# Optimization experiments

Hardware: AMD Instinct MI355X
Metric: run time of the kernel (lower is better)

Reference implementation:

```python
import jax, jax.numpy as jnp
import numpy as np

NC, NP, NF, NI, NIND = 150000, 300000, 100000, 700, 500
D, H, P = 64, 64, 32768


def setup_inputs() -> dict:
    key = jax.random.key(0)
    ks = jax.random.split(key, 40)

    def nrm(k, shape, s=0.05):
        return jax.random.normal(k, shape, dtype=jnp.float32) * s

    def idx(k, shape, hi):
        return jax.random.randint(k, shape, 0, hi, dtype=jnp.int32)

    def msk(k, shape):
        m = jax.random.bernoulli(k, 0.7, shape)
        return m.at[:, 0].set(True)  # guarantee >=1 neighbor per node

    inp = {
        # paths: columns are (company, patent, first_patentee, patent) for 'cpfp'
        "paths": jnp.stack([idx(ks[0], (P,), NC), idx(ks[1], (P,), NP),
                             idx(ks[2], (P,), NF), idx(ks[3], (P,), NP)], axis=1),
        "label": (jax.random.uniform(ks[4], (P,)) > 0.5).astype(jnp.float32),
        "pat_fp_idx": idx(ks[5], (NP, 2), NF),   "pat_fp_mask": msk(ks[6], (NP, 2)),
        "pat_ipc_idx": idx(ks[7], (NP, 6), NI),  "pat_ipc_mask": msk(ks[8], (NP, 6)),
        "pat_comp_idx": idx(ks[9], (NP, 2), NC), "pat_comp_mask": msk(ks[10], (NP, 2)),
        "comp_ind_idx": idx(ks[11], (NC, 4), NIND), "comp_ind_mask": msk(ks[12], (NC, 4)),
        "comp_pat_idx": idx(ks[13], (NC, 16), NP),  "comp_pat_mask": msk(ks[14], (NC, 16)),
        # embedding tables
        "company_emb": nrm(ks[15], (NC, D)),
        "patent_emb": nrm(ks[16], (NP, D)),
        "fp_emb": nrm(ks[17], (NF, D)),
        "ipc_emb": nrm(ks[18], (NI, D)),
        "ind_emb": nrm(ks[19], (NIND, D)),
        # LSTM (torch gate order i,f,g,o)
        "W_ih": nrm(ks[20], (4 * H, D)), "W_hh": nrm(ks[21], (4 * H, H)),
        "b_ih": jnp.zeros((4 * H,), jnp.float32), "b_hh": jnp.zeros((4 * H,), jnp.float32),
        # att_mlp: Linear(2D,D) -> LeakyReLU(0.2) -> Linear(D,1) -> Sigmoid
        "att_W1": nrm(ks[22], (2 * D, D)), "att_b1": jnp.zeros((D,), jnp.float32),
        "att_W2": nrm(ks[23], (D, 1)),     "att_b2": jnp.zeros((1,), jnp.float32),
        # score mlp: Linear(H,H) -> ReLU -> Linear(H,1) -> Sigmoid
        "mlp_W1": nrm(ks[24], (H, H)), "mlp_b1": jnp.zeros((H,), jnp.float32),
        "mlp_W2": nrm(ks[25], (H, 1)), "mlp_b2": jnp.zeros((1,), jnp.float32),
    }
    return inp


def _masked_sum(tab, idx, mask):
    # tab [V,D], idx [N,K], mask [N,K] bool -> (sum [N,D], count [N])
    e = tab[idx] * mask[..., None].astype(tab.dtype)
    return e.sum(1), mask.sum(1).astype(tab.dtype)


def _att_fuse(e, sub, W1, b1, W2, b2):
    # entity_embedding + subgraph * att_mlp([entity, subgraph])
    h = jax.nn.leaky_relu(jnp.concatenate([e, sub], -1) @ W1 + b1, 0.2)
    w = jax.nn.sigmoid(h @ W2 + b2)  # [P,1]
    return e + sub * w


def _lstm_last(seq, W_ih, W_hh, b_ih, b_hh):
    # seq [P,T,D] -> last hidden [P,H]
    h0 = jnp.zeros((seq.shape[0], H), seq.dtype)
    c0 = jnp.zeros_like(h0)

    def step(carry, x):
        h, c = carry
        g = x @ W_ih.T + b_ih + h @ W_hh.T + b_hh
        i, f, gg, o = jnp.split(g, 4, axis=-1)
        c = jax.nn.sigmoid(f) * c + jax.nn.sigmoid(i) * jnp.tanh(gg)
        h = jax.nn.sigmoid(o) * jnp.tanh(c)
        return (h, c), None

    (h, _), _ = jax.lax.scan(step, (h0, c0), jnp.swapaxes(seq, 0, 1))
    return h


def reference(paths, label, pat_fp_idx, pat_fp_mask, pat_ipc_idx, pat_ipc_mask,
              pat_comp_idx, pat_comp_mask, comp_ind_idx, comp_ind_mask,
              comp_pat_idx, comp_pat_mask, company_emb, patent_emb, fp_emb,
              ipc_emb, ind_emb, W_ih, W_hh, b_ih, b_hh, att_W1, att_b1,
              att_W2, att_b2, mlp_W1, mlp_b1, mlp_W2, mlp_b2):
    # --- compute_subgraph_representation (aggregator='avg'), vectorized ---
    s1, c1 = _masked_sum(fp_emb, pat_fp_idx, pat_fp_mask)
    s2, c2 = _masked_sum(ipc_emb, pat_ipc_idx, pat_ipc_mask)
    s3, c3 = _masked_sum(company_emb, pat_comp_idx, pat_comp_mask)
    patent_sub = patent_emb + (s1 + s2 + s3) / (c1 + c2 + c3)[:, None]  # [NP,D]

    t1, d1 = _masked_sum(ind_emb, comp_ind_idx, comp_ind_mask)
    t2, d2 = _masked_sum(patent_emb, comp_pat_idx, comp_pat_mask)
    company_sub = company_emb + (t1 + t2) / (d1 + d2)[:, None]          # [NC,D]

    # --- per-path entity embeddings for 'cpfp' ---
    e0 = company_emb[paths[:, 0]]
    e1 = patent_emb[paths[:, 1]]
    e2 = fp_emb[paths[:, 2]]
    e3 = patent_emb[paths[:, 3]]

    # fusion_type='att': fuse company subgraph (head) and patent subgraph (tail)
    # into intermediate entities (positions 1 and 2), sequentially.
    csub = company_sub[paths[:, 0]]
    psub = patent_sub[paths[:, 3]]
    e1 = _att_fuse(_att_fuse(e1, csub, att_W1, att_b1, att_W2, att_b2),
                   psub, att_W1, att_b1, att_W2, att_b2)
    e2 = _att_fuse(_att_fuse(e2, csub, att_W1, att_b1, att_W2, att_b2),
                   psub, att_W1, att_b1, att_W2, att_b2)

    seq = jnp.stack([e0, e1, e2, e3], axis=1)  # [P,4,D]
    h = _lstm_last(seq, W_ih, W_hh, b_ih, b_hh)  # [P,H]
    score = jax.nn.sigmoid(jax.nn.relu(h @ mlp_W1 + mlp_b1) @ mlp_W2 + mlp_b2)
    return score[:, 0]  # [P]
```

## Files before the change

kernel.cpp:

```cpp
#include <hip/hip_runtime.h>
#include <stdint.h>

typedef unsigned short u16;
typedef unsigned short u16x8 __attribute__((ext_vector_type(8)));
typedef short s16x8 __attribute__((ext_vector_type(8)));
typedef float f32x4 __attribute__((ext_vector_type(4)));

__device__ __forceinline__ float b2f(u16 u){ return __uint_as_float(((unsigned)u)<<16); }
__device__ __forceinline__ u16 f2b(float f){
  unsigned u = __float_as_uint(f);
  u += 0x7FFF + ((u>>16)&1);
  return (u16)(u>>16);
}
__device__ __forceinline__ float sigm(float x){ return 1.0f/(1.0f+__expf(-x)); }
__device__ __forceinline__ float tanhf_(float x){ return 2.0f/(1.0f+__expf(-2.0f*x)) - 1.0f; }

__device__ __forceinline__ f32x4 mf(s16x8 a, s16x8 b, f32x4 c){
  return __builtin_amdgcn_mfma_f32_16x16x32_bf16(a, b, c, 0, 0, 0);
}

__global__ void prep_kernel(const float* __restrict__ att_W1, const float* __restrict__ W_ih,
                            const float* __restrict__ W_hh, const float* __restrict__ mlp_W1,
                            u16* __restrict__ pack){
  int t = blockIdx.x*blockDim.x + threadIdx.x;
  if (t >= 5632) return;
  int lane = t & 63;
  int kb = (lane>>4)<<3;
  int nl = lane & 15;
  u16x8 o;
  if (t < 1024){
    int f = t>>6; int nt=f>>2, ks=f&3;
    int n = (nt<<4)+nl;
    #pragma unroll
    for (int j=0;j<8;j++){ int k = ks*32+kb+j; o[j] = f2b(att_W1[k*64+n]); }
  } else if (t < 3072){
    int f=(t-1024)>>6; int nt=f>>1, ks=f&1;
    int n=(nt<<4)+nl;
    #pragma unroll
    for (int j=0;j<8;j++){ int k=ks*32+kb+j; o[j]=f2b(W_ih[n*64+k]); }
  } else if (t < 5120){
    int f=(t-3072)>>6; int nt=f>>1, ks=f&1;
    int n=(nt<<4)+nl;
    #pragma unroll
    for (int j=0;j<8;j++){ int k=ks*32+kb+j; o[j]=f2b(W_hh[n*64+k]); }
  } else {
    int f=(t-5120)>>6; int nt=f>>1, ks=f&1;
    int n=(nt<<4)+nl;
    #pragma unroll
    for (int j=0;j<8;j++){ int k=ks*32+kb+j; o[j]=f2b(mlp_W1[k*64+n]); }
  }
  ((u16x8*)pack)[t] = o;
}

__global__ __launch_bounds__(256) void gather_kernel(
    const int* __restrict__ paths,
    const int* __restrict__ pat_fp_idx,  const uint8_t* __restrict__ pat_fp_mask,
    const int* __restrict__ pat_ipc_idx, const uint8_t* __restrict__ pat_ipc_mask,
    const int* __restrict__ pat_comp_idx,const uint8_t* __restrict__ pat_comp_mask,
    const int* __restrict__ comp_ind_idx,const uint8_t* __restrict__ comp_ind_mask,
    const int* __restrict__ comp_pat_idx,const uint8_t* __restrict__ comp_pat_mask,
    const float* __restrict__ company_emb, const float* __restrict__ patent_emb,
    const float* __restrict__ fp_emb, const float* __restrict__ ipc_emb,
    const float* __restrict__ ind_emb,
    u16* __restrict__ tileimg, int P, int total)
{
  const int lane = threadIdx.x & 63;
  const int p = (blockIdx.x<<2) + (threadIdx.x>>6);
  if (p >= total) return;
  const int ps = p < P ? p : (P-1);
  const int4 pq = *(const int4*)&paths[ps*4];

  int4   ci  = *(const int4*)  &comp_ind_idx [pq.x*4];
  const uchar4 cim = *(const uchar4*)&comp_ind_mask[pq.x*4];
  ci.y = cim.y ? ci.y : ci.x;  ci.z = cim.z ? ci.z : ci.x;  ci.w = cim.w ? ci.w : ci.x;

  int4   cp[4]; uchar4 cpm[4];
  #pragma unroll
  for (int q=0;q<4;q++){
    cp[q]  = *(const int4*)  &comp_pat_idx [pq.x*16+q*4];
    cpm[q] = *(const uchar4*)&comp_pat_mask[pq.x*16+q*4];
  }
  const int cp0 = cp[0].x;
  #pragma unroll
  for (int q=0;q<4;q++){
    cp[q].x = cpm[q].x ? cp[q].x : cp0;  cp[q].y = cpm[q].y ? cp[q].y : cp0;
    cp[q].z = cpm[q].z ? cp[q].z : cp0;  cp[q].w = cpm[q].w ? cp[q].w : cp0;
  }

  int2   fi  = *(const int2*)  &pat_fp_idx  [pq.w*2];
  const uchar2 fim = *(const uchar2*)&pat_fp_mask [pq.w*2];
  fi.y = fim.y ? fi.y : fi.x;

  int2   ip[3]; uchar2 ipm[3];
  #pragma unroll
  for (int q=0;q<3;q++){
    ip[q]  = *(const int2*)  &pat_ipc_idx [pq.w*6+q*2];
    ipm[q] = *(const uchar2*)&pat_ipc_mask[pq.w*6+q*2];
  }
  const int ip0 = ip[0].x;
  #pragma unroll
  for (int q=0;q<3;q++){
    ip[q].x = ipm[q].x ? ip[q].x : ip0;  ip[q].y = ipm[q].y ? ip[q].y : ip0;
  }

  int2   cc  = *(const int2*)  &pat_comp_idx [pq.w*2];
  const uchar2 ccm = *(const uchar2*)&pat_comp_mask[pq.w*2];
  cc.y = ccm.y ? cc.y : cc.x;

  const float e0 = company_emb[(long)pq.x*64+lane];
  const float e1 = patent_emb [(long)pq.y*64+lane];
  const float e2 = fp_emb     [(long)pq.z*64+lane];
  const float e3 = patent_emb [(long)pq.w*64+lane];

  float vind[4];
  vind[0]=ind_emb[(long)ci.x*64+lane]; vind[1]=ind_emb[(long)ci.y*64+lane];
  vind[2]=ind_emb[(long)ci.z*64+lane]; vind[3]=ind_emb[(long)ci.w*64+lane];
  float vpat[16];
  #pragma unroll
  for (int q=0;q<4;q++){
    vpat[q*4+0]=patent_emb[(long)cp[q].x*64+lane];
    vpat[q*4+1]=patent_emb[(long)cp[q].y*64+lane];
    vpat[q*4+2]=patent_emb[(long)cp[q].z*64+lane];
    vpat[q*4+3]=patent_emb[(long)cp[q].w*64+lane];
  }
  float vfp[2];
  vfp[0]=fp_emb[(long)fi.x*64+lane]; vfp[1]=fp_emb[(long)fi.y*64+lane];
  float vipc[6];
  #pragma unroll
  for (int q=0;q<3;q++){
    vipc[q*2+0]=ipc_emb[(long)ip[q].x*64+lane];
    vipc[q*2+1]=ipc_emb[(long)ip[q].y*64+lane];
  }
  float vcc[2];
  vcc[0]=company_emb[(long)cc.x*64+lane]; vcc[1]=company_emb[(long)cc.y*64+lane];

  float mi[4] = {(float)cim.x,(float)cim.y,(float)cim.z,(float)cim.w};
  float mp[16];
  #pragma unroll
  for (int q=0;q<4;q++){ mp[q*4]=(float)cpm[q].x; mp[q*4+1]=(float)cpm[q].y; mp[q*4+2]=(float)cpm[q].z; mp[q*4+3]=(float)cpm[q].w; }
  float a0=0.f, a1=0.f, c0=0.f, c1=0.f;
  #pragma unroll
  for (int j=0;j<4;j++){ a0 = fmaf(mi[j], vind[j], a0); c0 += mi[j]; }
  #pragma unroll
  for (int j=0;j<16;j++){
    if (j&1){ a1 = fmaf(mp[j], vpat[j], a1); c1 += mp[j]; }
    else    { a0 = fmaf(mp[j], vpat[j], a0); c0 += mp[j]; }
  }
  const float csub = e0 + (a0+a1)/(c0+c1);

  float mf2[2] = {(float)fim.x,(float)fim.y};
  float mip[6];
  #pragma unroll
  for (int q=0;q<3;q++){ mip[q*2]=(float)ipm[q].x; mip[q*2+1]=(float)ipm[q].y; }
  float mcc[2] = {(float)ccm.x,(float)ccm.y};
  float b0=0.f, b1=0.f, d0=0.f, d1=0.f;
  #pragma unroll
  for (int j=0;j<2;j++){ b0 = fmaf(mf2[j], vfp[j], b0); d0 += mf2[j]; }
  #pragma unroll
  for (int j=0;j<6;j++){
    if (j&1){ b1 = fmaf(mip[j], vipc[j], b1); d1 += mip[j]; }
    else    { b0 = fmaf(mip[j], vipc[j], b0); d0 += mip[j]; }
  }
  #pragma unroll
  for (int j=0;j<2;j++){ b1 = fmaf(mcc[j], vcc[j], b1); d1 += mcc[j]; }
  const float psub = e3 + (b0+b1)/(d0+d1);

  const int tile = p>>4, r = p&15;
  const int sc = lane ^ ((r&7)<<3);
  u16* b = tileimg + ((size_t)tile*6*16 + r)*64 + sc;
  b[0*1024] = f2b(e0);   b[1*1024] = f2b(e1);   b[2*1024] = f2b(e2);
  b[3*1024] = f2b(e3);   b[4*1024] = f2b(csub); b[5*1024] = f2b(psub);
}

__global__ __launch_bounds__(64) void path_kernel_fast(
    const float* __restrict__ b_ih, const float* __restrict__ b_hh,
    const float* __restrict__ att_b1, const float* __restrict__ att_W2, const float* __restrict__ att_b2,
    const float* __restrict__ mlp_b1, const float* __restrict__ mlp_W2, const float* __restrict__ mlp_b2,
    const u16* __restrict__ pack, const u16* __restrict__ tileimg,
    float* __restrict__ out, int P)
{
  __shared__ __align__(16) u16 ldsT[6][16][64];
  __shared__ float wbuf[32];
  const int lane = threadIdx.x;
  const int tile = blockIdx.x;
  const int base = tile * 16;
  if (base >= P) return;
  const u16x8* pk8 = (const u16x8*)pack;

  const char* src = (const char*)(tileimg + (size_t)tile*6144);
  #pragma unroll
  for (int it=0; it<12; ++it){
    __builtin_amdgcn_global_load_lds(
      (const __attribute__((address_space(1))) uint32_t*)(src + it*1024 + lane*16),
      (__attribute__((address_space(3))) uint32_t*)((char*)&ldsT[0][0][0] + it*1024),
      16, 0, 0);
  }
  asm volatile("s_waitcnt vmcnt(0)" ::: "memory");
  __builtin_amdgcn_sched_barrier(0);

  auto ldA = [&](int t, int ks)->s16x8{
    int row = lane & 15;
    int off = (ks*32 + ((lane>>4)<<3)) ^ ((row&7)<<3);
    return *(const s16x8*)&ldsT[t][row][off];
  };

  float attb1v[4], attw2v[4];
  #pragma unroll
  for (int q=0;q<4;q++){ int c=(q<<4)+(lane&15); attb1v[q]=att_b1[c]; attw2v[q]=att_W2[c]; }
  const float attb2 = att_b2[0];

  auto fuse = [&](int st){
    s16x8 a1[4], a2[4];
    #pragma unroll
    for (int ks=0;ks<2;ks++){
      a1[ks]=ldA(1,ks); a2[ks]=ldA(2,ks);
      s16x8 asub=ldA(st,ks); a1[2+ks]=asub; a2[2+ks]=asub;
    }
    f32x4 c1[4], c2[4];
    #pragma unroll
    for (int nt=0;nt<4;nt++){
      f32x4 x1={0.f,0.f,0.f,0.f}, x2={0.f,0.f,0.f,0.f};
      #pragma unroll
      for (int ks=0;ks<4;ks++){
        s16x8 b = *(const s16x8*)&pk8[(nt*4+ks)*64 + lane];
        x1 = mf(a1[ks], b, x1);
        x2 = mf(a2[ks], b, x2);
      }
      c1[nt]=x1; c2[nt]=x2;
    }
    float t1[4]={0.f,0.f,0.f,0.f}, t2[4]={0.f,0.f,0.f,0.f};
    #pragma unroll
    for (int nt=0;nt<4;nt++){
      #pragma unroll
      for (int r=0;r<4;r++){
        float h1=c1[nt][r]+attb1v[nt]; h1 = h1>0.f?h1:0.2f*h1;
        float h2=c2[nt][r]+attb1v[nt]; h2 = h2>0.f?h2:0.2f*h2;
        t1[r] += h1*attw2v[nt]; t2[r] += h2*attw2v[nt];
      }
    }
    #pragma unroll
    for (int r=0;r<4;r++){
      #pragma unroll
      for (int off=1; off<16; off<<=1){ t1[r]+=__shfl_xor(t1[r],off,64); t2[r]+=__shfl_xor(t2[r],off,64); }
    }
    if ((lane&15)==0){
      int g = lane>>4;
      #pragma unroll
      for (int r=0;r<4;r++){ wbuf[g*4+r] = sigm(t1[r]+attb2); wbuf[16+g*4+r] = sigm(t2[r]+attb2); }
    }
    #pragma unroll
    for (int it=0; it<2; it++){
      int row = it*8 + (lane>>3);
      int off = ((lane&7)<<3) ^ ((row&7)<<3);
      u16x8 ue1 = *(const u16x8*)&ldsT[1][row][off];
      u16x8 ue2 = *(const u16x8*)&ldsT[2][row][off];
      u16x8 us  = *(const u16x8*)&ldsT[st][row][off];
      float wA = wbuf[row], wB = wbuf[16+row];
      u16x8 o1, o2;
      #pragma unroll
      for (int j=0;j<8;j++){
        float sv=b2f(us[j]);
        o1[j]=f2b(b2f(ue1[j]) + sv*wA);
        o2[j]=f2b(b2f(ue2[j]) + sv*wB);
      }
      *(u16x8*)&ldsT[1][row][off]=o1;
      *(u16x8*)&ldsT[2][row][off]=o2;
    }
  };
  fuse(4);
  fuse(5);

  float biasv[16];
  #pragma unroll
  for (int nt=0;nt<16;nt++){ int c=(nt<<4)+(lane&15); biasv[nt]=b_ih[c]+b_hh[c]; }
  float cst[16];
  #pragma unroll
  for (int i=0;i<16;i++) cst[i]=0.f;

  auto step=[&](int xt, bool useH){
    s16x8 ax0=ldA(xt,0), ax1=ldA(xt,1);
    s16x8 ah0, ah1;
    if (useH){ ah0=ldA(4,0); ah1=ldA(4,1); }
    f32x4 acc[16];
    #pragma unroll
    for (int nt=0;nt<16;nt++){
      f32x4 a={0.f,0.f,0.f,0.f};
      a = mf(ax0, *(const s16x8*)&pk8[1024 + (nt*2+0)*64 + lane], a);
      a = mf(ax1, *(const s16x8*)&pk8[1024 + (nt*2+1)*64 + lane], a);
      if (useH){
        a = mf(ah0, *(const s16x8*)&pk8[3072 + (nt*2+0)*64 + lane], a);
        a = mf(ah1, *(const s16x8*)&pk8[3072 + (nt*2+1)*64 + lane], a);
      }
      acc[nt]=a;
    }
    #pragma unroll
    for (int q=0;q<4;q++){
      #pragma unroll
      for (int r=0;r<4;r++){
        float iv=sigm  (acc[q    ][r]+biasv[q]);
        float fv=sigm  (acc[4+q  ][r]+biasv[4+q]);
        float gv=tanhf_(acc[8+q  ][r]+biasv[8+q]);
        float ov=sigm  (acc[12+q ][r]+biasv[12+q]);
        float cc=fv*cst[q*4+r]+iv*gv;
        cst[q*4+r]=cc;
        float hv=ov*tanhf_(cc);
        int row=((lane>>4)<<2)+r;
        int col=(lane&15)+(q<<4);
        ldsT[4][row][col ^ ((row&7)<<3)] = f2b(hv);
      }
    }
  };
  step(0,false); step(1,true); step(2,true); step(3,true);

  float mlb1v[4], mlw2v[4];
  #pragma unroll
  for (int q=0;q<4;q++){ int c=(q<<4)+(lane&15); mlb1v[q]=mlp_b1[c]; mlw2v[q]=mlp_W2[c]; }
  const float mlb2 = mlp_b2[0];
  s16x8 ah0=ldA(4,0), ah1=ldA(4,1);
  f32x4 mac[4];
  #pragma unroll
  for (int nt=0;nt<4;nt++){
    f32x4 a={0.f,0.f,0.f,0.f};
    a = mf(ah0, *(const s16x8*)&pk8[5120 + (nt*2+0)*64 + lane], a);
    a = mf(ah1, *(const s16x8*)&pk8[5120 + (nt*2+1)*64 + lane], a);
    mac[nt]=a;
  }
  float tt[4]={0.f,0.f,0.f,0.f};
  #pragma unroll
  for (int nt=0;nt<4;nt++){
    #pragma unroll
    for (int r=0;r<4;r++){ float mv=mac[nt][r]+mlb1v[nt]; mv=mv>0.f?mv:0.f; tt[r]+=mv*mlw2v[nt]; }
  }
  #pragma unroll
  for (int r=0;r<4;r++){
    #pragma unroll
    for (int off=1; off<16; off<<=1) tt[r]+=__shfl_xor(tt[r],off,64);
  }
  if ((lane&15)==0){
    #pragma unroll
    for (int r=0;r<4;r++){
      int p = base + ((lane>>4)<<2) + r;
      if (p < P) out[p] = sigm(tt[r]+mlb2);
    }
  }
}

__global__ __launch_bounds__(64) void path_kernel_fused(
    const int* __restrict__ paths,
    const int* __restrict__ pat_fp_idx,  const uint8_t* __restrict__ pat_fp_mask,
    const int* __restrict__ pat_ipc_idx, const uint8_t* __restrict__ pat_ipc_mask,
    const int* __restrict__ pat_comp_idx,const uint8_t* __restrict__ pat_comp_mask,
    const int* __restrict__ comp_ind_idx,const uint8_t* __restrict__ comp_ind_mask,
    const int* __restrict__ comp_pat_idx,const uint8_t* __restrict__ comp_pat_mask,
    const float* __restrict__ company_emb, const float* __restrict__ patent_emb,
    const float* __restrict__ fp_emb, const float* __restrict__ ipc_emb,
    const float* __restrict__ ind_emb,
    const float* __restrict__ b_ih, const float* __restrict__ b_hh,
    const float* __restrict__ att_b1, const float* __restrict__ att_W2, const float* __restrict__ att_b2,
    const float* __restrict__ mlp_b1, const float* __restrict__ mlp_W2, const float* __restrict__ mlp_b2,
    const u16* __restrict__ pack,
    float* __restrict__ out, int P)
{
  __shared__ __align__(16) u16 ldsT[7][16][64];
  __shared__ float wbuf[32];
  const int lane = threadIdx.x;
  const int base = blockIdx.x * 16;
  if (base >= P) return;
  const u16x8* pk8 = (const u16x8*)pack;

  #pragma unroll 2
  for (int r=0;r<16;r++){
    int p = base + r; int ps = p < P ? p : (P-1);
    const int4 pq = *(const int4*)&paths[ps*4];
    float e0 = company_emb[(long)pq.x*64+lane];
    float e1 = patent_emb [(long)pq.y*64+lane];
    float e2 = fp_emb     [(long)pq.z*64+lane];
    float e3 = patent_emb [(long)pq.w*64+lane];
    float acc=0.f, cnt=0.f;
    #pragma unroll
    for (int jj=0;jj<4;jj++)
      if (comp_ind_mask[pq.x*4+jj]) { acc += ind_emb[(long)comp_ind_idx[pq.x*4+jj]*64+lane]; cnt += 1.f; }
    #pragma unroll
    for (int jj=0;jj<16;jj++)
      if (comp_pat_mask[pq.x*16+jj]){ acc += patent_emb[(long)comp_pat_idx[pq.x*16+jj]*64+lane]; cnt += 1.f; }
    float csub = e0 + acc/cnt;
    acc=0.f; cnt=0.f;
    #pragma unroll
    for (int jj=0;jj<2;jj++)
      if (pat_fp_mask[pq.w*2+jj])  { acc += fp_emb[(long)pat_fp_idx[pq.w*2+jj]*64+lane]; cnt += 1.f; }
    #pragma unroll
    for (int jj=0;jj<6;jj++)
      if (pat_ipc_mask[pq.w*6+jj]) { acc += ipc_emb[(long)pat_ipc_idx[pq.w*6+jj]*64+lane]; cnt += 1.f; }
    #pragma unroll
    for (int jj=0;jj<2;jj++)
      if (pat_comp_mask[pq.w*2+jj]){ acc += company_emb[(long)pat_comp_idx[pq.w*2+jj]*64+lane]; cnt += 1.f; }
    float psub = e3 + acc/cnt;
    int sc = lane ^ ((r&7)<<3);
    ldsT[0][r][sc]=f2b(e0); ldsT[1][r][sc]=f2b(e1); ldsT[2][r][sc]=f2b(e2);
    ldsT[3][r][sc]=f2b(e3); ldsT[4][r][sc]=f2b(csub); ldsT[5][r][sc]=f2b(psub);
  }

  auto ldA = [&](int t, int ks)->s16x8{
    int row = lane & 15;
    int off = (ks*32 + ((lane>>4)<<3)) ^ ((row&7)<<3);
    return *(const s16x8*)&ldsT[t][row][off];
  };

  float attb1v[4], attw2v[4];
  #pragma unroll
  for (int q=0;q<4;q++){ int c=(q<<4)+(lane&15); attb1v[q]=att_b1[c]; attw2v[q]=att_W2[c]; }
  const float attb2 = att_b2[0];

  auto fuse = [&](int st){
    s16x8 a1[4], a2[4];
    #pragma unroll
    for (int ks=0;ks<2;ks++){
      a1[ks]=ldA(1,ks); a2[ks]=ldA(2,ks);
      s16x8 asub=ldA(st,ks); a1[2+ks]=asub; a2[2+ks]=asub;
    }
    f32x4 c1[4], c2[4];
    #pragma unroll
    for (int nt=0;nt<4;nt++){
      f32x4 x1={0.f,0.f,0.f,0.f}, x2={0.f,0.f,0.f,0.f};
      #pragma unroll
      for (int ks=0;ks<4;ks++){
        s16x8 b = *(const s16x8*)&pk8[(nt*4+ks)*64 + lane];
        x1 = mf(a1[ks], b, x1);
        x2 = mf(a2[ks], b, x2);
      }
      c1[nt]=x1; c2[nt]=x2;
    }
    float t1[4]={0.f,0.f,0.f,0.f}, t2[4]={0.f,0.f,0.f,0.f};
    #pragma unroll
    for (int nt=0;nt<4;nt++){
      #pragma unroll
      for (int r=0;r<4;r++){
        float h1=c1[nt][r]+attb1v[nt]; h1 = h1>0.f?h1:0.2f*h1;
        float h2=c2[nt][r]+attb1v[nt]; h2 = h2>0.f?h2:0.2f*h2;
        t1[r] += h1*attw2v[nt]; t2[r] += h2*attw2v[nt];
      }
    }
    #pragma unroll
    for (int r=0;r<4;r++){
      #pragma unroll
      for (int off=1; off<16; off<<=1){ t1[r]+=__shfl_xor(t1[r],off,64); t2[r]+=__shfl_xor(t2[r],off,64); }
    }
    if ((lane&15)==0){
      int g = lane>>4;
      #pragma unroll
      for (int r=0;r<4;r++){ wbuf[g*4+r] = sigm(t1[r]+attb2); wbuf[16+g*4+r] = sigm(t2[r]+attb2); }
    }
    #pragma unroll
    for (int it=0; it<2; it++){
      int row = it*8 + (lane>>3);
      int off = ((lane&7)<<3) ^ ((row&7)<<3);
      u16x8 ue1 = *(const u16x8*)&ldsT[1][row][off];
      u16x8 ue2 = *(const u16x8*)&ldsT[2][row][off];
      u16x8 us  = *(const u16x8*)&ldsT[st][row][off];
      float wA = wbuf[row], wB = wbuf[16+row];
      u16x8 o1, o2;
      #pragma unroll
      for (int j=0;j<8;j++){
        float sv=b2f(us[j]);
        o1[j]=f2b(b2f(ue1[j]) + sv*wA);
        o2[j]=f2b(b2f(ue2[j]) + sv*wB);
      }
      *(u16x8*)&ldsT[1][row][off]=o1;
      *(u16x8*)&ldsT[2][row][off]=o2;
    }
  };
  fuse(4); fuse(5);

  float biasv[16];
  #pragma unroll
  for (int nt=0;nt<16;nt++){ int c=(nt<<4)+(lane&15); biasv[nt]=b_ih[c]+b_hh[c]; }
  float cst[16];
  #pragma unroll
  for (int i=0;i<16;i++) cst[i]=0.f;

  auto step=[&](int xt, bool useH){
    s16x8 ax0=ldA(xt,0), ax1=ldA(xt,1);
    s16x8 ah0, ah1;
    if (useH){ ah0=ldA(6,0); ah1=ldA(6,1); }
    f32x4 acc[16];
    #pragma unroll
    for (int nt=0;nt<16;nt++){
      f32x4 a={0.f,0.f,0.f,0.f};
      a = mf(ax0, *(const s16x8*)&pk8[1024 + (nt*2+0)*64 + lane], a);
      a = mf(ax1, *(const s16x8*)&pk8[1024 + (nt*2+1)*64 + lane], a);
      if (useH){
        a = mf(ah0, *(const s16x8*)&pk8[3072 + (nt*2+0)*64 + lane], a);
        a = mf(ah1, *(const s16x8*)&pk8[3072 + (nt*2+1)*64 + lane], a);
      }
      acc[nt]=a;
    }
    #pragma unroll
    for (int q=0;q<4;q++){
      #pragma unroll
      for (int r=0;r<4;r++){
        float iv=sigm  (acc[q    ][r]+biasv[q]);
        float fv=sigm  (acc[4+q  ][r]+biasv[4+q]);
        float gv=tanhf_(acc[8+q  ][r]+biasv[8+q]);
        float ov=sigm  (acc[12+q ][r]+biasv[12+q]);
        float cc=fv*cst[q*4+r]+iv*gv;
        cst[q*4+r]=cc;
        float hv=ov*tanhf_(cc);
        int row=((lane>>4)<<2)+r;
        int col=(lane&15)+(q<<4);
        ldsT[6][row][col ^ ((row&7)<<3)] = f2b(hv);
      }
    }
  };
  step(0,false); step(1,true); step(2,true); step(3,true);

  float mlb1v[4], mlw2v[4];
  #pragma unroll
  for (int q=0;q<4;q++){ int c=(q<<4)+(lane&15); mlb1v[q]=mlp_b1[c]; mlw2v[q]=mlp_W2[c]; }
  const float mlb2 = mlp_b2[0];
  s16x8 ah0=ldA(6,0), ah1=ldA(6,1);
  f32x4 mac[4];
  #pragma unroll
  for (int nt=0;nt<4;nt++){
    f32x4 a={0.f,0.f,0.f,0.f};
    a = mf(ah0, *(const s16x8*)&pk8[5120 + (nt*2+0)*64 + lane], a);
    a = mf(ah1, *(const s16x8*)&pk8[5120 + (nt*2+1)*64 + lane], a);
    mac[nt]=a;
  }
  float tt[4]={0.f,0.f,0.f,0.f};
  #pragma unroll
  for (int nt=0;nt<4;nt++){
    #pragma unroll
    for (int r=0;r<4;r++){ float mv=mac[nt][r]+mlb1v[nt]; mv=mv>0.f?mv:0.f; tt[r]+=mv*mlw2v[nt]; }
  }
  #pragma unroll
  for (int r=0;r<4;r++){
    #pragma unroll
    for (int off=1; off<16; off<<=1) tt[r]+=__shfl_xor(tt[r],off,64);
  }
  if ((lane&15)==0){
    #pragma unroll
    for (int r=0;r<4;r++){
      int p = base + ((lane>>4)<<2) + r;
      if (p < P) out[p] = sigm(tt[r]+mlb2);
    }
  }
}

extern "C" void kernel_launch(void* const* d_in, const int* in_sizes, int n_in,
                              void* d_out, int out_size, void* d_ws, size_t ws_size,
                              hipStream_t stream){
  const int*     paths         = (const int*)    d_in[0];
  const int*     pat_fp_idx    = (const int*)    d_in[2];
  const uint8_t* pat_fp_mask   = (const uint8_t*)d_in[3];
  const int*     pat_ipc_idx   = (const int*)    d_in[4];
  const uint8_t* pat_ipc_mask  = (const uint8_t*)d_in[5];
  const int*     pat_comp_idx  = (const int*)    d_in[6];
  const uint8_t* pat_comp_mask = (const uint8_t*)d_in[7];
  const int*     comp_ind_idx  = (const int*)    d_in[8];
  const uint8_t* comp_ind_mask = (const uint8_t*)d_in[9];
  const int*     comp_pat_idx  = (const int*)    d_in[10];
  const uint8_t* comp_pat_mask = (const uint8_t*)d_in[11];
  const float*   company_emb   = (const float*)  d_in[12];
  const float*   patent_emb    = (const float*)  d_in[13];
  const float*   fp_emb        = (const float*)  d_in[14];
  const float*   ipc_emb       = (const float*)  d_in[15];
  const float*   ind_emb       = (const float*)  d_in[16];
  const float*   W_ih          = (const float*)  d_in[17];
  const float*   W_hh          = (const float*)  d_in[18];
  const float*   b_ih          = (const float*)  d_in[19];
  const float*   b_hh          = (const float*)  d_in[20];
  const float*   att_W1        = (const float*)  d_in[21];
  const float*   att_b1        = (const float*)  d_in[22];
  const float*   att_W2        = (const float*)  d_in[23];
  const float*   att_b2        = (const float*)  d_in[24];
  const float*   mlp_W1        = (const float*)  d_in[25];
  const float*   mlp_b1        = (const float*)  d_in[26];
  const float*   mlp_W2        = (const float*)  d_in[27];
  const float*   mlp_b2        = (const float*)  d_in[28];
  float* out = (float*)d_out;
  const int P = in_sizes[1];

  u16* pack = (u16*)d_ws;
  const size_t packB = 5632u * 16u;
  const int tiles = (P + 15) / 16;
  const int total = tiles * 16;
  const size_t need = packB + (size_t)tiles * 12288u;

  prep_kernel<<<22, 256, 0, stream>>>(att_W1, W_ih, W_hh, mlp_W1, pack);

  if (ws_size >= need){
    u16* tileimg = (u16*)((char*)d_ws + packB);
    gather_kernel<<<tiles*4, 256, 0, stream>>>(
        paths,
        pat_fp_idx, pat_fp_mask, pat_ipc_idx, pat_ipc_mask, pat_comp_idx, pat_comp_mask,
        comp_ind_idx, comp_ind_mask, comp_pat_idx, comp_pat_mask,
        company_emb, patent_emb, fp_emb, ipc_emb, ind_emb,
        tileimg, P, total);
    path_kernel_fast<<<tiles, 64, 0, stream>>>(
        b_ih, b_hh, att_b1, att_W2, att_b2,
        mlp_b1, mlp_W2, mlp_b2,
        pack, tileimg, out, P);
  } else {
    path_kernel_fused<<<tiles, 64, 0, stream>>>(
        paths,
        pat_fp_idx, pat_fp_mask, pat_ipc_idx, pat_ipc_mask, pat_comp_idx, pat_comp_mask,
        comp_ind_idx, comp_ind_mask, comp_pat_idx, comp_pat_mask,
        company_emb, patent_emb, fp_emb, ipc_emb, ind_emb,
        b_ih, b_hh, att_b1, att_W2, att_b2,
        mlp_b1, mlp_W2, mlp_b2,
        pack, out, P);
  }
}
```

Before: 76.65 us.

## Process two path tiles per wavefront in path_kernel_fast to reuse weight fragments

Each 64-thread block now handles two 16-path tiles, loading both tile images into a doubled LDS buffer. Every weight fragment read from the packed global buffer feeds MFMAs for both tiles, which halves weight loads per path and gives the scheduler two independent MFMA chains to interleave. The LSTM step is reorganised per gate quarter so fewer accumulators are live at once. The cost is half as many blocks (2048 to 1024 for P=32768), more LDS and registers per wave, and so possibly lower occupancy and less latency hiding.

```diff
diff --git a/kernel.cpp b/kernel.cpp
--- a/kernel.cpp
+++ b/kernel.cpp
@@ -177,31 +177,39 @@
     const float* __restrict__ att_b1, const float* __restrict__ att_W2, const float* __restrict__ att_b2,
     const float* __restrict__ mlp_b1, const float* __restrict__ mlp_W2, const float* __restrict__ mlp_b2,
     const u16* __restrict__ pack, const u16* __restrict__ tileimg,
-    float* __restrict__ out, int P)
+    float* __restrict__ out, int P, int tiles)
 {
-  __shared__ __align__(16) u16 ldsT[6][16][64];
-  __shared__ float wbuf[32];
+  __shared__ __align__(16) u16 ldsT[2][6][16][64];
+  __shared__ float wbuf[2][32];
   const int lane = threadIdx.x;
-  const int tile = blockIdx.x;
-  const int base = tile * 16;
-  if (base >= P) return;
+  const int t0 = blockIdx.x * 2;
+  if (t0 >= tiles) return;
+  const int t1s = (t0+1 < tiles) ? (t0+1) : t0;
   const u16x8* pk8 = (const u16x8*)pack;
 
-  const char* src = (const char*)(tileimg + (size_t)tile*6144);
+  const char* s0 = (const char*)(tileimg + (size_t)t0 *6144);
+  const char* s1 = (const char*)(tileimg + (size_t)t1s*6144);
   #pragma unroll
   for (int it=0; it<12; ++it){
     __builtin_amdgcn_global_load_lds(
-      (const __attribute__((address_space(1))) uint32_t*)(src + it*1024 + lane*16),
-      (__attribute__((address_space(3))) uint32_t*)((char*)&ldsT[0][0][0] + it*1024),
+      (const __attribute__((address_space(1))) uint32_t*)(s0 + it*1024 + lane*16),
+      (__attribute__((address_space(3))) uint32_t*)((char*)&ldsT[0][0][0][0] + it*1024),
+      16, 0, 0);
+  }
+  #pragma unroll
+  for (int it=0; it<12; ++it){
+    __builtin_amdgcn_global_load_lds(
+      (const __attribute__((address_space(1))) uint32_t*)(s1 + it*1024 + lane*16),
+      (__attribute__((address_space(3))) uint32_t*)((char*)&ldsT[1][0][0][0] + it*1024),
       16, 0, 0);
   }
   asm volatile("s_waitcnt vmcnt(0)" ::: "memory");
   __builtin_amdgcn_sched_barrier(0);
 
-  auto ldA = [&](int t, int ks)->s16x8{
+  auto ldA = [&](int tl, int t, int ks)->s16x8{
     int row = lane & 15;
     int off = (ks*32 + ((lane>>4)<<3)) ^ ((row&7)<<3);
-    return *(const s16x8*)&ldsT[t][row][off];
+    return *(const s16x8*)&ldsT[tl][t][row][off];
   };
 
   float attb1v[4], attw2v[4];
@@ -210,62 +218,83 @@
   const float attb2 = att_b2[0];
 
   auto fuse = [&](int st){
-    s16x8 a1[4], a2[4];
-    #pragma unroll
-    for (int ks=0;ks<2;ks++){
-      a1[ks]=ldA(1,ks); a2[ks]=ldA(2,ks);
-      s16x8 asub=ldA(st,ks); a1[2+ks]=asub; a2[2+ks]=asub;
-    }
-    f32x4 c1[4], c2[4];
-    #pragma unroll
-    for (int nt=0;nt<4;nt++){
-      f32x4 x1={0.f,0.f,0.f,0.f}, x2={0.f,0.f,0.f,0.f};
-      #pragma unroll
-      for (int ks=0;ks<4;ks++){
+    s16x8 fe1[2][2], fe2[2][2], fs[2][2];
+    #pragma unroll
+    for (int tl=0; tl<2; ++tl)
+      #pragma unroll
+      for (int ks=0; ks<2; ++ks){
+        fe1[tl][ks]=ldA(tl,1,ks); fe2[tl][ks]=ldA(tl,2,ks); fs[tl][ks]=ldA(tl,st,ks);
+      }
+    float t1[2][4], t2[2][4];
+    #pragma unroll
+    for (int tl=0; tl<2; ++tl)
+      #pragma unroll
+      for (int r=0;r<4;r++){ t1[tl][r]=0.f; t2[tl][r]=0.f; }
+    #pragma unroll
+    for (int nt=0; nt<4; ++nt){
+      f32x4 x1[2], x2[2];
+      #pragma unroll
+      for (int tl=0; tl<2; ++tl){ x1[tl]=(f32x4){0.f,0.f,0.f,0.f}; x2[tl]=(f32x4){0.f,0.f,0.f,0.f}; }
+      #pragma unroll
+      for (int ks=0; ks<4; ++ks){
         s16x8 b = *(const s16x8*)&pk8[(nt*4+ks)*64 + lane];
-        x1 = mf(a1[ks], b, x1);
-        x2 = mf(a2[ks], b, x2);
-      }
-      c1[nt]=x1; c2[nt]=x2;
-    }
-    float t1[4]={0.f,0.f,0.f,0.f}, t2[4]={0.f,0.f,0.f,0.f};
-    #pragma unroll
-    for (int nt=0;nt<4;nt++){
+        #pragma unroll
+        for (int tl=0; tl<2; ++tl){
+          s16x8 aa = (ks<2) ? fe1[tl][ks] : fs[tl][ks-2];
+          s16x8 bb = (ks<2) ? fe2[tl][ks] : fs[tl][ks-2];
+          x1[tl] = mf(aa, b, x1[tl]);
+          x2[tl] = mf(bb, b, x2[tl]);
+        }
+      }
+      #pragma unroll
+      for (int tl=0; tl<2; ++tl)
+        #pragma unroll
+        for (int r=0;r<4;r++){
+          float h1=x1[tl][r]+attb1v[nt]; h1 = h1>0.f?h1:0.2f*h1;
+          float h2=x2[tl][r]+attb1v[nt]; h2 = h2>0.f?h2:0.2f*h2;
+          t1[tl][r] += h1*attw2v[nt]; t2[tl][r] += h2*attw2v[nt];
+        }
+    }
+    #pragma unroll
+    for (int tl=0; tl<2; ++tl)
       #pragma unroll
       for (int r=0;r<4;r++){
-        float h1=c1[nt][r]+attb1v[nt]; h1 = h1>0.f?h1:0.2f*h1;
-        float h2=c2[nt][r]+attb1v[nt]; h2 = h2>0.f?h2:0.2f*h2;
-        t1[r] += h1*attw2v[nt]; t2[r] += h2*attw2v[nt];
-      }
-    }
-    #pragma unroll
-    for (int r=0;r<4;r++){
-      #pragma unroll
-      for (int off=1; off<16; off<<=1){ t1[r]+=__shfl_xor(t1[r],off,64); t2[r]+=__shfl_xor(t2[r],off,64); }
-    }
+        #pragma unroll
+        for (int off=1; off<16; off<<=1){
+          t1[tl][r]+=__shfl_xor(t1[tl][r],off,64);
+          t2[tl][r]+=__shfl_xor(t2[tl][r],off,64);
+        }
+      }
     if ((lane&15)==0){
       int g = lane>>4;
       #pragma unroll
-      for (int r=0;r<4;r++){ wbuf[g*4+r] = sigm(t1[r]+attb2); wbuf[16+g*4+r] = sigm(t2[r]+attb2); }
-    }
-    #pragma unroll
-    for (int it=0; it<2; it++){
-      int row = it*8 + (lane>>3);
-      int off = ((lane&7)<<3) ^ ((row&7)<<3);
-      u16x8 ue1 = *(const u16x8*)&ldsT[1][row][off];
-      u16x8 ue2 = *(const u16x8*)&ldsT[2][row][off];
-      u16x8 us  = *(const u16x8*)&ldsT[st][row][off];
-      float wA = wbuf[row], wB = wbuf[16+row];
-      u16x8 o1, o2;
-      #pragma unroll
-      for (int j=0;j<8;j++){
-        float sv=b2f(us[j]);
-        o1[j]=f2b(b2f(ue1[j]) + sv*wA);
-        o2[j]=f2b(b2f(ue2[j]) + sv*wB);
-      }
-      *(u16x8*)&ldsT[1][row][off]=o1;
-      *(u16x8*)&ldsT[2][row][off]=o2;
-    }
+      for (int tl=0; tl<2; ++tl)
+        #pragma unroll
+        for (int r=0;r<4;r++){
+          wbuf[tl][g*4+r] = sigm(t1[tl][r]+attb2);
+          wbuf[tl][16+g*4+r] = sigm(t2[tl][r]+attb2);
+        }
+    }
+    #pragma unroll
+    for (int tl=0; tl<2; ++tl)
+      #pragma unroll
+      for (int it=0; it<2; it++){
+        int row = it*8 + (lane>>3);
+        int off = ((lane&7)<<3) ^ ((row&7)<<3);
+        u16x8 ue1 = *(const u16x8*)&ldsT[tl][1][row][off];
+        u16x8 ue2 = *(const u16x8*)&ldsT[tl][2][row][off];
+        u16x8 us  = *(const u16x8*)&ldsT[tl][st][row][off];
+        float wA = wbuf[tl][row], wB = wbuf[tl][16+row];
+        u16x8 o1, o2;
+        #pragma unroll
+        for (int j=0;j<8;j++){
+          float sv=b2f(us[j]);
+          o1[j]=f2b(b2f(ue1[j]) + sv*wA);
+          o2[j]=f2b(b2f(ue2[j]) + sv*wB);
+        }
+        *(u16x8*)&ldsT[tl][1][row][off]=o1;
+        *(u16x8*)&ldsT[tl][2][row][off]=o2;
+      }
   };
   fuse(4);
   fuse(5);
@@ -273,41 +302,61 @@
   float biasv[16];
   #pragma unroll
   for (int nt=0;nt<16;nt++){ int c=(nt<<4)+(lane&15); biasv[nt]=b_ih[c]+b_hh[c]; }
-  float cst[16];
-  #pragma unroll
-  for (int i=0;i<16;i++) cst[i]=0.f;
+  float cst[2][16];
+  #pragma unroll
+  for (int tl=0; tl<2; ++tl)
+    #pragma unroll
+    for (int i=0;i<16;i++) cst[tl][i]=0.f;
 
   auto step=[&](int xt, bool useH){
-    s16x8 ax0=ldA(xt,0), ax1=ldA(xt,1);
-    s16x8 ah0, ah1;
-    if (useH){ ah0=ldA(4,0); ah1=ldA(4,1); }
-    f32x4 acc[16];
-    #pragma unroll
-    for (int nt=0;nt<16;nt++){
-      f32x4 a={0.f,0.f,0.f,0.f};
-      a = mf(ax0, *(const s16x8*)&pk8[1024 + (nt*2+0)*64 + lane], a);
-      a = mf(ax1, *(const s16x8*)&pk8[1024 + (nt*2+1)*64 + lane], a);
-      if (useH){
-        a = mf(ah0, *(const s16x8*)&pk8[3072 + (nt*2+0)*64 + lane], a);
-        a = mf(ah1, *(const s16x8*)&pk8[3072 + (nt*2+1)*64 + lane], a);
-      }
-      acc[nt]=a;
+    s16x8 fx[2][2], fh[2][2];
+    #pragma unroll
+    for (int tl=0; tl<2; ++tl){
+      fx[tl][0]=ldA(tl,xt,0); fx[tl][1]=ldA(tl,xt,1);
+      if (useH){ fh[tl][0]=ldA(tl,4,0); fh[tl][1]=ldA(tl,4,1); }
     }
     #pragma unroll
     for (int q=0;q<4;q++){
-      #pragma unroll
-      for (int r=0;r<4;r++){
-        float iv=sigm  (acc[q    ][r]+biasv[q]);
-        float fv=sigm  (acc[4+q  ][r]+biasv[4+q]);
-        float gv=tanhf_(acc[8+q  ][r]+biasv[8+q]);
-        float ov=sigm  (acc[12+q ][r]+biasv[12+q]);
-        float cc=fv*cst[q*4+r]+iv*gv;
-        cst[q*4+r]=cc;
-        float hv=ov*tanhf_(cc);
-        int row=((lane>>4)<<2)+r;
-        int col=(lane&15)+(q<<4);
-        ldsT[4][row][col ^ ((row&7)<<3)] = f2b(hv);
-      }
+      f32x4 acc[2][4];
+      #pragma unroll
+      for (int tl=0; tl<2; ++tl)
+        #pragma unroll
+        for (int g=0; g<4; ++g) acc[tl][g]=(f32x4){0.f,0.f,0.f,0.f};
+      #pragma unroll
+      for (int g=0; g<4; ++g){
+        int nt = g*4+q;
+        s16x8 b0 = *(const s16x8*)&pk8[1024 + (nt*2+0)*64 + lane];
+        s16x8 b1 = *(const s16x8*)&pk8[1024 + (nt*2+1)*64 + lane];
+        #pragma unroll
+        for (int tl=0; tl<2; ++tl){
+          acc[tl][g] = mf(fx[tl][0], b0, acc[tl][g]);
+          acc[tl][g] = mf(fx[tl][1], b1, acc[tl][g]);
+        }
+        if (useH){
+          s16x8 b2 = *(const s16x8*)&pk8[3072 + (nt*2+0)*64 + lane];
+          s16x8 b3 = *(const s16x8*)&pk8[3072 + (nt*2+1)*64 + lane];
+          #pragma unroll
+          for (int tl=0; tl<2; ++tl){
+            acc[tl][g] = mf(fh[tl][0], b2, acc[tl][g]);
+            acc[tl][g] = mf(fh[tl][1], b3, acc[tl][g]);
+          }
+        }
+      }
+      #pragma unroll
+      for (int tl=0; tl<2; ++tl)
+        #pragma unroll
+        for (int r=0;r<4;r++){
+          float iv=sigm  (acc[tl][0][r]+biasv[q]);
+          float fv=sigm  (acc[tl][1][r]+biasv[4+q]);
+          float gv=tanhf_(acc[tl][2][r]+biasv[8+q]);
+          float ov=sigm  (acc[tl][3][r]+biasv[12+q]);
+          float ccv=fv*cst[tl][q*4+r]+iv*gv;
+          cst[tl][q*4+r]=ccv;
+          float hv=ov*tanhf_(ccv);
+          int row=((lane>>4)<<2)+r;
+          int col=(lane&15)+(q<<4);
+          ldsT[tl][4][row][col ^ ((row&7)<<3)] = f2b(hv);
+        }
     }
   };
   step(0,false); step(1,true); step(2,true); step(3,true);
@@ -316,31 +365,43 @@
   #pragma unroll
   for (int q=0;q<4;q++){ int c=(q<<4)+(lane&15); mlb1v[q]=mlp_b1[c]; mlw2v[q]=mlp_W2[c]; }
   const float mlb2 = mlp_b2[0];
-  s16x8 ah0=ldA(4,0), ah1=ldA(4,1);
-  f32x4 mac[4];
+  s16x8 gh[2][2];
+  #pragma unroll
+  for (int tl=0; tl<2; ++tl){ gh[tl][0]=ldA(tl,4,0); gh[tl][1]=ldA(tl,4,1); }
+  float tt[2][4];
+  #pragma unroll
+  for (int tl=0; tl<2; ++tl)
+    #pragma unroll
+    for (int r=0;r<4;r++) tt[tl][r]=0.f;
   #pragma unroll
   for (int nt=0;nt<4;nt++){
-    f32x4 a={0.f,0.f,0.f,0.f};
-    a = mf(ah0, *(const s16x8*)&pk8[5120 + (nt*2+0)*64 + lane], a);
-    a = mf(ah1, *(const s16x8*)&pk8[5120 + (nt*2+1)*64 + lane], a);
-    mac[nt]=a;
-  }
-  float tt[4]={0.f,0.f,0.f,0.f};
-  #pragma unroll
-  for (int nt=0;nt<4;nt++){
-    #pragma unroll
-    for (int r=0;r<4;r++){ float mv=mac[nt][r]+mlb1v[nt]; mv=mv>0.f?mv:0.f; tt[r]+=mv*mlw2v[nt]; }
-  }
-  #pragma unroll
-  for (int r=0;r<4;r++){
-    #pragma unroll
-    for (int off=1; off<16; off<<=1) tt[r]+=__shfl_xor(tt[r],off,64);
-  }
+    s16x8 b0 = *(const s16x8*)&pk8[5120 + (nt*2+0)*64 + lane];
+    s16x8 b1 = *(const s16x8*)&pk8[5120 + (nt*2+1)*64 + lane];
+    #pragma unroll
+    for (int tl=0; tl<2; ++tl){
+      f32x4 a={0.f,0.f,0.f,0.f};
+      a = mf(gh[tl][0], b0, a);
+      a = mf(gh[tl][1], b1, a);
+      #pragma unroll
+      for (int r=0;r<4;r++){ float mv=a[r]+mlb1v[nt]; mv=mv>0.f?mv:0.f; tt[tl][r]+=mv*mlw2v[nt]; }
+    }
+  }
+  #pragma unroll
+  for (int tl=0; tl<2; ++tl)
+    #pragma unroll
+    for (int r=0;r<4;r++){
+      #pragma unroll
+      for (int off=1; off<16; off<<=1) tt[tl][r]+=__shfl_xor(tt[tl][r],off,64);
+    }
   if ((lane&15)==0){
     #pragma unroll
-    for (int r=0;r<4;r++){
-      int p = base + ((lane>>4)<<2) + r;
-      if (p < P) out[p] = sigm(tt[r]+mlb2);
+    for (int tl=0; tl<2; ++tl){
+      int base = (t0+tl)*16;
+      #pragma unroll
+      for (int r=0;r<4;r++){
+        int p = base + ((lane>>4)<<2) + r;
+        if (p < P) out[p] = sigm(tt[tl][r]+mlb2);
+      }
     }
   }
 }
@@ -596,10 +657,11 @@
         comp_ind_idx, comp_ind_mask, comp_pat_idx, comp_pat_mask,
         company_emb, patent_emb, fp_emb, ipc_emb, ind_emb,
         tileimg, P, total);
-    path_kernel_fast<<<tiles, 64, 0, stream>>>(
+    int blocks2 = (tiles + 1) / 2;
+    path_kernel_fast<<<blocks2, 64, 0, stream>>>(
         b_ih, b_hh, att_b1, att_W2, att_b2,
         mlp_b1, mlp_W2, mlp_b2,
-        pack, tileimg, out, P);
+        pack, tileimg, out, P, tiles);
   } else {
     path_kernel_fused<<<tiles, 64, 0, stream>>>(
         paths,
```

New measurement: 100.3 us. 30.8% more time.
